# Kernel tuning notes

Hardware: AMD Instinct MI355X
Metric: run time of the kernel (lower is better)

The kernel has to match this reference:

```python
import jax, jax.numpy as jnp
import numpy as np

N_EMBD = 384
HEAD_SIZE = 64
BLOCK_SIZE = 64
SCALE = HEAD_SIZE * N_EMBD ** (-0.5)  # non-standard scale from source: k.shape[-1] * C**-0.5


def setup_inputs() -> dict:
    key = jax.random.key(0)
    kx, kk, kq, kv = jax.random.split(key, 4)
    B, T = 2048, BLOCK_SIZE
    x = jax.random.normal(kx, (B, T, N_EMBD), dtype=jnp.float32)
    # torch Linear(n_embd, head_size, bias=False): weight shape [head_size, n_embd], y = x @ W.T
    s = N_EMBD ** -0.5
    Wk = jax.random.uniform(kk, (HEAD_SIZE, N_EMBD), jnp.float32, -s, s)
    Wq = jax.random.uniform(kq, (HEAD_SIZE, N_EMBD), jnp.float32, -s, s)
    Wv = jax.random.uniform(kv, (HEAD_SIZE, N_EMBD), jnp.float32, -s, s)
    return {"x": x, "Wk": Wk, "Wq": Wq, "Wv": Wv}


def reference(x, Wk, Wq, Wv) -> jnp.ndarray:
    B, T, C = x.shape
    k = jnp.einsum("btc,hc->bth", x, Wk)  # [B,T,H]
    q = jnp.einsum("btc,hc->bth", x, Wq)
    v = jnp.einsum("btc,hc->bth", x, Wv)
    wei = jnp.einsum("bth,bsh->bts", q, k) * SCALE  # [B,T,T]
    causal = jnp.tril(jnp.ones((T, T), dtype=bool))
    wei = jnp.where(causal, wei, -jnp.inf)
    wei = jax.nn.softmax(wei, axis=-1)
    out = jnp.einsum("bts,bsh->bth", wei, v)  # [B,T,H]
    return out
```

## Files before the change

### kernel.cpp

```cpp
#include <hip/hip_runtime.h>

typedef _Float16 f16;
typedef _Float16 f16x8 __attribute__((ext_vector_type(8)));
typedef _Float16 f16x4 __attribute__((ext_vector_type(4)));
typedef float    f32x4 __attribute__((ext_vector_type(4)));

#define MFMA16(a, b, c) __builtin_amdgcn_mfma_f32_16x16x32_f16((a), (b), (c), 0, 0, 0)

constexpr int T = 64;
constexpr int C = 384;
constexpr int H = 64;
constexpr float SCALE = 3.26598632371090f;

__global__ void pack_w(const float* __restrict__ Wk, const float* __restrict__ Wq,
                       const float* __restrict__ Wv, f16* __restrict__ Wp) {
  int tid = blockIdx.x * blockDim.x + threadIdx.x;
  if (tid >= 3 * 12 * 4 * 64) return;
  int lane = tid & 63;
  int tile = tid >> 6;
  int ht = tile & 3;
  int kt = (tile >> 2) % 12;
  int wi = tile / 48;
  const float* W = (wi == 0) ? Wk : ((wi == 1) ? Wq : Wv);
  int h = 16 * ht + (lane & 15);
  int c = 32 * kt + 8 * (lane >> 4);
  const float* src = W + h * C + c;
  f16x8 v;
#pragma unroll
  for (int j = 0; j < 8; ++j) v[j] = (f16)src[j];
  *(f16x8*)(Wp + (size_t)tile * 512 + lane * 8) = v;
}

__global__ __launch_bounds__(256, 4) void head_fused(
    const float* __restrict__ x, const f16* __restrict__ Wp,
    float* __restrict__ out) {
  __shared__ f16 qp_lds[64][72];
  __shared__ f16 k_lds[64][72];
  __shared__ f16 vT_lds[64][72];

  const int b = blockIdx.x;
  const int tid = threadIdx.x;
  const int w = tid >> 6;
  const int lane = tid & 63;
  const int l15 = lane & 15;
  const int g = lane >> 4;
  const int t_ = 16 * w + l15;

  const f32x4 vzero = {0.0f, 0.0f, 0.0f, 0.0f};
  f32x4 acc[3][4];
#pragma unroll
  for (int c = 0; c < 3; ++c)
#pragma unroll
    for (int tt = 0; tt < 4; ++tt) acc[c][tt] = vzero;

  const f16* wp_base[3];
  bool isV[3];
#pragma unroll
  for (int c = 0; c < 3; ++c) {
    int combo = 3 * w + c;
    int m = combo >> 2;
    int ht = combo & 3;
    wp_base[c] = Wp + (size_t)(m * 48 + ht) * 512 + lane * 8;
    isV[c] = (combo >= 8);
  }

  const float* xbase = x + (size_t)b * T * C;

#pragma unroll
  for (int kt = 0; kt < 12; ++kt) {
    f16x8 xf[4];
#pragma unroll
    for (int tt = 0; tt < 4; ++tt) {
      const float* xr = xbase + (size_t)(16 * tt + l15) * C + kt * 32 + g * 8;
      f32x4 a0 = *(const f32x4*)(xr);
      f32x4 a1 = *(const f32x4*)(xr + 4);
#pragma unroll
      for (int j = 0; j < 4; ++j) { xf[tt][j] = (f16)a0[j]; xf[tt][4 + j] = (f16)a1[j]; }
    }
#pragma unroll
    for (int c = 0; c < 3; ++c) {
      f16x8 wf = *(const f16x8*)(wp_base[c] + kt * 2048);
      if (!isV[c]) {
#pragma unroll
        for (int tt = 0; tt < 4; ++tt) acc[c][tt] = MFMA16(wf, xf[tt], acc[c][tt]);
      } else {
#pragma unroll
        for (int tt = 0; tt < 4; ++tt) acc[c][tt] = MFMA16(xf[tt], wf, acc[c][tt]);
      }
    }
  }

#pragma unroll
  for (int c = 0; c < 3; ++c) {
    int combo = 3 * w + c;
    int m = combo >> 2;
    int ht = combo & 3;
#pragma unroll
    for (int tt = 0; tt < 4; ++tt) {
      f16x4 pd;
#pragma unroll
      for (int r = 0; r < 4; ++r) pd[r] = (f16)acc[c][tt][r];
      if (m == 0) {
        *(f16x4*)&k_lds[16 * tt + l15][16 * ht + 4 * g] = pd;
      } else if (m == 1) {
        *(f16x4*)&qp_lds[16 * tt + l15][16 * ht + 4 * g] = pd;
      } else {
        *(f16x4*)&vT_lds[16 * ht + l15][16 * tt + 4 * g] = pd;
      }
    }
  }
  __syncthreads();

  f32x4 accs[4];
#pragma unroll
  for (int i = 0; i < 4; ++i) accs[i] = vzero;
#pragma unroll
  for (int kt = 0; kt < 2; ++kt) {
    f16x8 qf = *(const f16x8*)&qp_lds[t_][32 * kt + 8 * g];
#pragma unroll
    for (int mt = 0; mt < 4; ++mt) {
      f16x8 kf = *(const f16x8*)&k_lds[16 * mt + l15][32 * kt + 8 * g];
      accs[mt] = MFMA16(kf, qf, accs[mt]);
    }
  }

  float e[16];
  float mx = -__builtin_inff();
#pragma unroll
  for (int mt = 0; mt < 4; ++mt) {
#pragma unroll
    for (int r = 0; r < 4; ++r) {
      int s = 16 * mt + 4 * g + r;
      float lv = accs[mt][r] * SCALE;
      lv = (s <= t_) ? lv : -__builtin_inff();
      e[mt * 4 + r] = lv;
      mx = fmaxf(mx, lv);
    }
  }
  mx = fmaxf(mx, __shfl_xor(mx, 16));
  mx = fmaxf(mx, __shfl_xor(mx, 32));
  float sm = 0.0f;
#pragma unroll
  for (int i = 0; i < 16; ++i) { e[i] = __expf(e[i] - mx); sm += e[i]; }
  sm += __shfl_xor(sm, 16);
  sm += __shfl_xor(sm, 32);
  const float inv = 1.0f / sm;
#pragma unroll
  for (int mt = 0; mt < 4; ++mt) {
    f16x4 pp;
#pragma unroll
    for (int r = 0; r < 4; ++r) pp[r] = (f16)(e[mt * 4 + r] * inv);
    *(f16x4*)&qp_lds[t_][16 * mt + 4 * g] = pp;
  }

  f32x4 acco[4];
#pragma unroll
  for (int i = 0; i < 4; ++i) acco[i] = vzero;
#pragma unroll
  for (int kt = 0; kt < 2; ++kt) {
    f16x8 pf = *(const f16x8*)&qp_lds[t_][32 * kt + 8 * g];
#pragma unroll
    for (int mt = 0; mt < 4; ++mt) {
      f16x8 vf = *(const f16x8*)&vT_lds[16 * mt + l15][32 * kt + 8 * g];
      acco[mt] = MFMA16(vf, pf, acco[mt]);
    }
  }

  float* orow = out + ((size_t)b * T + t_) * H;
#pragma unroll
  for (int mt = 0; mt < 4; ++mt) {
    *(f32x4*)(orow + 16 * mt + 4 * g) = acco[mt];
  }
}

extern "C" void kernel_launch(void* const* d_in, const int* in_sizes, int n_in,
                              void* d_out, int out_size, void* d_ws, size_t ws_size,
                              hipStream_t stream) {
  const float* x  = (const float*)d_in[0];
  const float* Wk = (const float*)d_in[1];
  const float* Wq = (const float*)d_in[2];
  const float* Wv = (const float*)d_in[3];
  float* out = (float*)d_out;
  f16* Wp = (f16*)d_ws;

  pack_w<<<36, 256, 0, stream>>>(Wk, Wq, Wv, Wp);
  head_fused<<<2048, 256, 0, stream>>>(x, Wp, out);
}
```

Measured before the change: 334.6 us.

## Double-buffer x tiles in LDS via global_load_lds and prefetch weights

Replaces direct per-wave global loads of x (each of 4 waves redundantly reading all 64 rows) with cooperative async global-to-LDS loads into a double buffer, so each wave loads only its 16 rows per k-step. Weight fragments are prefetched one iteration ahead in registers. This cuts redundant global traffic and overlaps loads with MFMA work, at the cost of 16KB extra LDS, two barriers per k-step, and a lower occupancy hint (3 blocks per CU).

```diff
diff --git a/kernel.cpp b/kernel.cpp
--- a/kernel.cpp
+++ b/kernel.cpp
@@ -11,6 +11,12 @@
 constexpr int C = 384;
 constexpr int H = 64;
 constexpr float SCALE = 3.26598632371090f;
+
+__device__ __forceinline__ void load_lds16(const float* g, float* l) {
+  __builtin_amdgcn_global_load_lds(
+      (const __attribute__((address_space(1))) void*)g,
+      (__attribute__((address_space(3))) void*)l, 16, 0, 0);
+}
 
 __global__ void pack_w(const float* __restrict__ Wk, const float* __restrict__ Wq,
                        const float* __restrict__ Wv, f16* __restrict__ Wp) {
@@ -31,9 +37,10 @@
   *(f16x8*)(Wp + (size_t)tile * 512 + lane * 8) = v;
 }
 
-__global__ __launch_bounds__(256, 4) void head_fused(
+__global__ __launch_bounds__(256, 3) void head_fused(
     const float* __restrict__ x, const f16* __restrict__ Wp,
     float* __restrict__ out) {
+  __shared__ float xc[2][2048];
   __shared__ f16 qp_lds[64][72];
   __shared__ f16 k_lds[64][72];
   __shared__ f16 vT_lds[64][72];
@@ -65,21 +72,38 @@
   }
 
   const float* xbase = x + (size_t)b * T * C;
-
-#pragma unroll
+  const float* gsrc = xbase + (size_t)(16 * w + l15) * C + g * 8;
+
+  load_lds16(gsrc + 0 * 32 + 0, &xc[0][(2 * w + 0) * 256]);
+  load_lds16(gsrc + 0 * 32 + 4, &xc[0][(2 * w + 1) * 256]);
+  f16x8 wpc[3], wpn[3];
+#pragma unroll
+  for (int c = 0; c < 3; ++c) wpc[c] = *(const f16x8*)(wp_base[c]);
+
+#pragma unroll 2
   for (int kt = 0; kt < 12; ++kt) {
+    const int cur = kt & 1;
+    if (kt + 1 < 12) {
+      load_lds16(gsrc + (kt + 1) * 32 + 0, &xc[cur ^ 1][(2 * w + 0) * 256]);
+      load_lds16(gsrc + (kt + 1) * 32 + 4, &xc[cur ^ 1][(2 * w + 1) * 256]);
+#pragma unroll
+      for (int c = 0; c < 3; ++c)
+        wpn[c] = *(const f16x8*)(wp_base[c] + (size_t)(kt + 1) * 2048);
+    }
+    __builtin_amdgcn_s_waitcnt(0x0f70);
+    __syncthreads();
+
     f16x8 xf[4];
 #pragma unroll
     for (int tt = 0; tt < 4; ++tt) {
-      const float* xr = xbase + (size_t)(16 * tt + l15) * C + kt * 32 + g * 8;
-      f32x4 a0 = *(const f32x4*)(xr);
-      f32x4 a1 = *(const f32x4*)(xr + 4);
-#pragma unroll
-      for (int j = 0; j < 4; ++j) { xf[tt][j] = (f16)a0[j]; xf[tt][4 + j] = (f16)a1[j]; }
+      f32x4 A0 = *(const f32x4*)&xc[cur][(2 * tt + 0) * 256 + lane * 4];
+      f32x4 A1 = *(const f32x4*)&xc[cur][(2 * tt + 1) * 256 + lane * 4];
+#pragma unroll
+      for (int j = 0; j < 4; ++j) { xf[tt][j] = (f16)A0[j]; xf[tt][4 + j] = (f16)A1[j]; }
     }
 #pragma unroll
     for (int c = 0; c < 3; ++c) {
-      f16x8 wf = *(const f16x8*)(wp_base[c] + kt * 2048);
+      f16x8 wf = wpc[c];
       if (!isV[c]) {
 #pragma unroll
         for (int tt = 0; tt < 4; ++tt) acc[c][tt] = MFMA16(wf, xf[tt], acc[c][tt]);
@@ -87,7 +111,9 @@
 #pragma unroll
         for (int tt = 0; tt < 4; ++tt) acc[c][tt] = MFMA16(xf[tt], wf, acc[c][tt]);
       }
-    }
+      wpc[c] = wpn[c];
+    }
+    __syncthreads();
   }
 
 #pragma unroll
```

After: 304.9 us. 1.1x faster.
